# Optimization experiments

Hardware: AMD Instinct MI355X
Metric: run time of the kernel (lower is better)

Reference implementation:

```python
import math
import jax, jax.numpy as jnp
import numpy as np

N_HEADS = 16
D_KV = 64
NUM_BUCKETS = 32
MAX_DISTANCE = 128


def _relative_position_bucket(relative_position, num_buckets=NUM_BUCKETS, max_distance=MAX_DISTANCE):
    # bidirectional=True (encoder)
    num_buckets //= 2
    n = -relative_position
    ret = (n < 0).astype(jnp.int32) * num_buckets
    n = jnp.abs(n)
    max_exact = num_buckets // 2
    is_small = n < max_exact
    val_if_large = max_exact + (
        jnp.log(jnp.maximum(n, 1).astype(jnp.float32) / max_exact)
        / math.log(max_distance / max_exact)
        * (num_buckets - max_exact)
    ).astype(jnp.int32)
    val_if_large = jnp.minimum(val_if_large, num_buckets - 1)
    return ret + jnp.where(is_small, n, val_if_large)


def setup_inputs() -> dict:
    key = jax.random.key(0)
    ks = jax.random.split(key, 6)
    B, S, D = 2, 2048, 1024
    scale = 0.02  # keep pre-softmax logits in a sane range
    return {
        "x": jax.random.normal(ks[0], (B, S, D), dtype=jnp.float32),
        "Wq": jax.random.normal(ks[1], (D, N_HEADS * D_KV), dtype=jnp.float32) * scale,
        "Wk": jax.random.normal(ks[2], (D, N_HEADS * D_KV), dtype=jnp.float32) * scale,
        "Wv": jax.random.normal(ks[3], (D, N_HEADS * D_KV), dtype=jnp.float32) * scale,
        "Wo": jax.random.normal(ks[4], (N_HEADS * D_KV, D), dtype=jnp.float32) * scale,
        "rel_emb": jax.random.normal(ks[5], (NUM_BUCKETS, N_HEADS), dtype=jnp.float32) * scale,
    }


def reference(x, Wq, Wk, Wv, Wo, rel_emb):
    B, S, D = x.shape
    H, Dk = N_HEADS, D_KV

    def shape(t):  # [B,S,H*Dk] -> [B,H,S,Dk]
        return t.reshape(B, S, H, Dk).transpose(0, 2, 1, 3)

    q = shape(x @ Wq)
    k = shape(x @ Wk)
    v = shape(x @ Wv)

    # NOTE: T5 attention has NO 1/sqrt(d) scaling.
    scores = jnp.einsum("bhqd,bhkd->bhqk", q, k)

    # relative position bias: [1, H, S, S]
    ctx_pos = jnp.arange(S)[:, None]
    mem_pos = jnp.arange(S)[None, :]
    rp_bucket = _relative_position_bucket(mem_pos - ctx_pos)  # [S, S]
    position_bias = rel_emb[rp_bucket].transpose(2, 0, 1)[None]  # [1,H,S,S]

    weights = jax.nn.softmax(scores + position_bias, axis=-1)
    context = jnp.einsum("bhqk,bhkd->bhqd", weights, v)
    context = context.transpose(0, 2, 1, 3).reshape(B, S, H * Dk)
    return context @ Wo
```

## Files before the change

### kernel.cpp

```cpp
#include <hip/hip_runtime.h>
#include <math.h>

typedef unsigned short u16;
typedef unsigned int u32;
typedef __attribute__((ext_vector_type(8))) short bf16x8_t;
typedef __attribute__((ext_vector_type(4))) float f32x4_t;
typedef __attribute__((ext_vector_type(16))) float f32x16_t;

#define S_LEN  2048
#define NH     16
#define DK     64
#define DMODEL 1024
#define MROWS  4096
#define LOG2E  1.44269504088896f

__device__ inline u16 f2b(float f) {
  union { float f; u32 u; } c; c.f = f;
  u32 u = c.u;
  return (u16)((u + 0x7fffu + ((u >> 16) & 1u)) >> 16);
}

__device__ __forceinline__ float fexp2(float x) {
#if __has_builtin(__builtin_amdgcn_exp2f)
  return __builtin_amdgcn_exp2f(x);
#else
  return exp2f(x);
#endif
}

__device__ __forceinline__ u32 cvtpk(float lo, float hi) {
  u32 r;
  asm("v_cvt_pk_bf16_f32 %0, %1, %2" : "=v"(r) : "v"(lo), "v"(hi));
  return r;
}

__device__ __forceinline__ void plswap(u32 &x, u32 &y) {
  asm("v_permlane32_swap_b32 %0, %1" : "+v"(x), "+v"(y));
}

__device__ __forceinline__ void stage16(const u16* gp_lane, u16* lds_base) {
#if __has_builtin(__builtin_amdgcn_global_load_lds)
  __builtin_amdgcn_global_load_lds((const __attribute__((address_space(1))) u32*)gp_lane,
                                   (__attribute__((address_space(3))) u32*)lds_base, 16, 0, 0);
#else
  *(uint4*)(lds_base + (threadIdx.x & 63) * 8) = *(const uint4*)gp_lane;
#endif
}

__global__ void prep_kernel(const float* __restrict__ x,
                            const float* __restrict__ Wq, const float* __restrict__ Wk,
                            const float* __restrict__ Wv, const float* __restrict__ Wo,
                            const float* __restrict__ rel,
                            u16* __restrict__ xb, u16* __restrict__ Wall,
                            u16* __restrict__ Wto, float* __restrict__ btab) {
  __shared__ float tile[32][33];
  const int bid = blockIdx.x, t = threadIdx.x;
  if (bid < 4096) {
    int i = (bid * 256 + t) * 4;
    float4 v = *(const float4*)(x + i);
    ushort4 o;
    o.x = f2b(v.x); o.y = f2b(v.y); o.z = f2b(v.z); o.w = f2b(v.w);
    *(ushort4*)(xb + i) = o;
  } else if (bid < 8192) {
    int bid2 = bid - 4096;
    int z = bid2 >> 10, rem = bid2 & 1023;
    const float* W; u16* Wt;
    switch (z) {
      case 0: W = Wq; Wt = Wall; break;
      case 1: W = Wk; Wt = Wall + (size_t)DMODEL * DMODEL; break;
      case 2: W = Wv; Wt = Wall + (size_t)2 * DMODEL * DMODEL; break;
      default: W = Wo; Wt = Wto; break;
    }
    int bc = (rem & 31) * 32, br = (rem >> 5) * 32;
    int tx = t & 31, ty = t >> 5;
    #pragma unroll
    for (int yy = 0; yy < 32; yy += 8)
      tile[ty + yy][tx] = W[(size_t)(br + ty + yy) * DMODEL + bc + tx];
    __syncthreads();
    #pragma unroll
    for (int yy = 0; yy < 32; yy += 8)
      Wt[(size_t)(bc + ty + yy) * DMODEL + br + tx] = f2b(tile[tx][ty + yy]);
  } else {
    int idx = (bid - 8192) * 256 + t;
    if (idx < NH * 4095) {
      int h = idx / 4095;
      int dpos = idx - h * 4095;
      int delta = dpos - 2047;
      int ret = (delta > 0) ? 16 : 0;
      int n = delta < 0 ? -delta : delta;
      int bucket;
      if (n < 8) {
        bucket = ret + n;
      } else {
        float vf = logf((float)n * 0.125f) / 2.7725887222397811f * 8.0f;
        int vil = 8 + (int)vf;
        bucket = ret + (vil < 15 ? vil : 15);
      }
      btab[idx] = (rel[bucket * NH + h] - 16.0f) * LOG2E;
    }
  }
}

#define GSTR 56
template <int MODE>
__global__ __launch_bounds__(256) void gemm128_kernel(const u16* __restrict__ A,
                                                      const u16* __restrict__ Bt,
                                                      float* __restrict__ C,
                                                      u16* __restrict__ q16,
                                                      u16* __restrict__ k16,
                                                      u16* __restrict__ vt16) {
  constexpr int ABSZ = (MODE == 1) ? 4608 : 128 * GSTR;
  constexpr int FSTR = (MODE == 1) ? 32 : GSTR;
  __shared__ __align__(16) u16 As[ABSZ];
  __shared__ __align__(16) u16 Bs[ABSZ];
  const int t = threadIdx.x, w = t >> 6, l = t & 63;
  const int c = l & 15, quad = l >> 4;
  const int m0 = blockIdx.x * 128, n0 = blockIdx.y * 128;
  const int wm = (w & 1) * 64, wn = (w >> 1) * 64;

  f32x4_t acc[16] = {};

  if constexpr (MODE == 1) {
    const int sr = l >> 2;
    const int k8 = (l & 3) * 8;
    const u16* Ag0 = A  + (size_t)(m0 + w * 32 + sr) * DMODEL + k8;
    const u16* Ag1 = Ag0 + (size_t)16 * DMODEL;
    const u16* Bg0 = Bt + (size_t)(n0 + w * 32 + sr) * DMODEL + k8;
    const u16* Bg1 = Bg0 + (size_t)16 * DMODEL;
    u16* Al = As + w * 1024;
    u16* Bl = Bs + w * 1024;
    for (int k0 = 0; k0 < DMODEL; k0 += 32) {
      __syncthreads();
      stage16(Ag0 + k0, Al);
      stage16(Ag1 + k0, Al + 512);
      stage16(Bg0 + k0, Bl);
      stage16(Bg1 + k0, Bl + 512);
      __syncthreads();
      bf16x8_t af[4], bfr[4];
      #pragma unroll
      for (int i = 0; i < 4; ++i) {
        af[i]  = *(const bf16x8_t*)(As + (wm + i * 16 + c) * FSTR + quad * 8);
        bfr[i] = *(const bf16x8_t*)(Bs + (wn + i * 16 + c) * FSTR + quad * 8);
      }
      #pragma unroll
      for (int mt = 0; mt < 4; ++mt)
        #pragma unroll
        for (int nt = 0; nt < 4; ++nt)
          acc[mt * 4 + nt] = __builtin_amdgcn_mfma_f32_16x16x32_bf16(af[mt], bfr[nt], acc[mt * 4 + nt], 0, 0, 0);
    }
  } else {
    const int sr = t >> 2;
    const int k8 = (t & 3) * 8;
    const u16* Ag0 = A  + (size_t)(m0 + sr) * DMODEL + k8;
    const u16* Ag1 = Ag0 + (size_t)64 * DMODEL;
    const u16* Bg0 = Bt + (size_t)(n0 + sr) * DMODEL + k8;
    const u16* Bg1 = Bg0 + (size_t)64 * DMODEL;
    u16* Al0 = As + sr * GSTR + k8;
    u16* Al1 = Al0 + 64 * GSTR;
    u16* Bl0 = Bs + sr * GSTR + k8;
    u16* Bl1 = Bl0 + 64 * GSTR;

    uint4 a0 = *(const uint4*)Ag0, a1 = *(const uint4*)Ag1;
    uint4 b0 = *(const uint4*)Bg0, b1 = *(const uint4*)Bg1;
    for (int k0 = 0; k0 < DMODEL; k0 += 32) {
      __syncthreads();
      *(uint4*)Al0 = a0; *(uint4*)Al1 = a1;
      *(uint4*)Bl0 = b0; *(uint4*)Bl1 = b1;
      __syncthreads();
      if (k0 + 32 < DMODEL) {
        a0 = *(const uint4*)(Ag0 + k0 + 32);
        a1 = *(const uint4*)(Ag1 + k0 + 32);
        b0 = *(const uint4*)(Bg0 + k0 + 32);
        b1 = *(const uint4*)(Bg1 + k0 + 32);
      }
      bf16x8_t af[4], bfr[4];
      #pragma unroll
      for (int i = 0; i < 4; ++i) {
        af[i]  = *(const bf16x8_t*)(As + (wm + i * 16 + c) * FSTR + quad * 8);
        bfr[i] = *(const bf16x8_t*)(Bs + (wn + i * 16 + c) * FSTR + quad * 8);
      }
      #pragma unroll
      for (int mt = 0; mt < 4; ++mt)
        #pragma unroll
        for (int nt = 0; nt < 4; ++nt)
          acc[mt * 4 + nt] = __builtin_amdgcn_mfma_f32_16x16x32_bf16(af[mt], bfr[nt], acc[mt * 4 + nt], 0, 0, 0);
    }
  }

  if constexpr (MODE == 0) {
    #pragma unroll
    for (int mt = 0; mt < 4; ++mt) {
      int grow0 = m0 + wm + mt * 16 + quad * 4;
      #pragma unroll
      for (int nt = 0; nt < 4; ++nt) {
        int gcol = n0 + wn + nt * 16 + c;
        #pragma unroll
        for (int r = 0; r < 4; ++r)
          C[(size_t)(grow0 + r) * DMODEL + gcol] = acc[mt * 4 + nt][r];
      }
    }
  } else {
    const int whichblk = n0 >> 10;
    if (whichblk == 2) {
      #pragma unroll
      for (int mt = 0; mt < 4; ++mt) {
        int grow0 = m0 + wm + mt * 16 + quad * 4;
        int b = grow0 >> 11, s0 = grow0 & 2047;
        #pragma unroll
        for (int nt = 0; nt < 4; ++nt) {
          int cc = (n0 + wn + nt * 16 + c) & 1023;
          int hh = cc >> 6, dk = cc & 63;
          f32x4_t v4 = acc[mt * 4 + nt];
          ushort4 o;
          o.x = f2b(v4[0]); o.y = f2b(v4[1]); o.z = f2b(v4[2]); o.w = f2b(v4[3]);
          *(ushort4*)(vt16 + (((size_t)(b * NH + hh)) * DK + dk) * S_LEN + s0) = o;
        }
      }
    } else {
      u16* tb = (w & 1) ? Bs : As;
      const int base_mw = m0 + wm;
      const int bb = base_mw >> 11, s0g = base_mw & 2047;
      const int cc = (n0 + wn) & 1023;
      const int hh = cc >> 6;
      u16* qk = (whichblk == 0 ? q16 : k16) + (((size_t)(bb * NH + hh)) * S_LEN + s0g) * DK;
      __syncthreads();
      #pragma unroll
      for (int round = 0; round < 2; ++round) {
        if ((w >> 1) == round) {
          #pragma unroll
          for (int mt = 0; mt < 4; ++mt)
            #pragma unroll
            for (int nt = 0; nt < 4; ++nt)
              #pragma unroll
              for (int r = 0; r < 4; ++r)
                tb[(mt * 16 + quad * 4 + r) * 72 + nt * 16 + c] = f2b(acc[mt * 4 + nt][r]);
          #pragma unroll
          for (int i = 0; i < 8; ++i) {
            int lrow = i * 8 + (l >> 3);
            int chk = l & 7;
            uint4 vv = *(const uint4*)(tb + lrow * 72 + chk * 8);
            *(uint4*)(qk + (size_t)lrow * DK + chk * 8) = vv;
          }
        }
        __syncthreads();
      }
    }
  }
}

#define KSTR 72
#define VSTR 136
__global__ __launch_bounds__(512, 4) void attn_mfma_kernel(const u16* __restrict__ q,
                                                           const u16* __restrict__ k,
                                                           const u16* __restrict__ vt,
                                                           const float* __restrict__ btab,
                                                           u16* __restrict__ ctx) {
  __shared__ __align__(16) char smem[37376];
  u16*   Ks   = (u16*)smem;
  u16*   Vts  = (u16*)(smem + 18432);
  float* band = (float*)(smem + 35840);
  float* lpx  = (float*)(smem + 36864);

  const int t = threadIdx.x;
  const int w = t >> 6, l = t & 63;
  const int c32 = l & 31, h32 = l >> 5;
  const int grp = w >> 1, kh = w & 1;

  const int orig = blockIdx.x;
  const int swz = (orig & 7) * 64 + (orig >> 3);
  const int bh = swz >> 4;
  const int q0 = (swz & 15) * 128;
  const int h = bh & (NH - 1), b = bh >> 4;

  const u16* qb = q + (size_t)bh * S_LEN * DK;
  const u16* kb = k + (size_t)bh * S_LEN * DK;
  const u16* vb = vt + (size_t)bh * DK * S_LEN;
  const float* btp = btab + h * 4095 + (2047 - 127 - q0);

  bf16x8_t qfrag[4];
  {
    const u16* qp = qb + (size_t)(q0 + grp * 32 + c32) * DK + h32 * 8;
    qfrag[0] = *(const bf16x8_t*)(qp);
    qfrag[1] = *(const bf16x8_t*)(qp + 16);
    qfrag[2] = *(const bf16x8_t*)(qp + 32);
    qfrag[3] = *(const bf16x8_t*)(qp + 48);
  }

  float lp = 0.f;
  f32x16_t O0 = {}, O1 = {};

  const int ksr = t >> 2;
  const int ksc = (t & 3) * 8;
  const u16* kgp = kb + (size_t)ksr * DK + ksc;
  u16* Kl = Ks + ksr * KSTR + ksc;
  const int vsr = t >> 3;
  const int vsc = (t & 7) * 8;
  const u16* vgp = vb + (size_t)vsr * S_LEN + vsc;
  u16* Vl = Vts + vsr * VSTR + vsc;

  uint4 kr0 = *(const uint4*)kgp;
  uint4 kr1 = *(const uint4*)(kgp + 32);
  uint4 vr0 = *(const uint4*)vgp;
  uint4 vr1 = *(const uint4*)(vgp + 64);
  float br = (t < 256) ? btp[t] : 0.f;

  const int krA = (kh * 64 + c32) * KSTR + h32 * 8;
  const int bndcA = 127 + kh * 64 + 4 * h32 - grp * 32 - c32;

  for (int kt = 0; kt < S_LEN; kt += 128) {
    *(uint4*)Kl = kr0;        *(uint4*)(Kl + 32) = kr1;
    *(uint4*)Vl = vr0;        *(uint4*)(Vl + 64) = vr1;
    if (t < 256) band[t] = br;
    __syncthreads();
    if (kt + 128 < S_LEN) {
      kr0 = *(const uint4*)(kgp + (size_t)(kt + 128) * DK);
      kr1 = *(const uint4*)(kgp + (size_t)(kt + 128) * DK + 32);
      vr0 = *(const uint4*)(vgp + (kt + 128));
      vr1 = *(const uint4*)(vgp + (kt + 128) + 64);
      br = (t < 256) ? btp[kt + 128 + t] : 0.f;
    }
    const int D = kt - q0;
    const bool far = (D >= 256) || (D <= -256);

    f32x16_t sA = {}, sB = {};
    __builtin_amdgcn_s_setprio(1);
    #pragma unroll
    for (int kb4 = 0; kb4 < 4; ++kb4) {
      bf16x8_t kfA = *(const bf16x8_t*)(Ks + krA + kb4 * 16);
      sA = __builtin_amdgcn_mfma_f32_32x32x16_bf16(kfA, qfrag[kb4], sA, 0, 0, 0);
    }
    #pragma unroll
    for (int kb4 = 0; kb4 < 4; ++kb4) {
      bf16x8_t kfB = *(const bf16x8_t*)(Ks + krA + 32 * KSTR + kb4 * 16);
      sB = __builtin_amdgcn_mfma_f32_32x32x16_bf16(kfB, qfrag[kb4], sB, 0, 0, 0);
    }
    __builtin_amdgcn_s_setprio(0);

    const float bfc = band[127];

    {
      float p[16];
      if (far) {
        #pragma unroll
        for (int r = 0; r < 16; ++r)
          p[r] = fexp2(fmaf(sA[r], LOG2E, bfc));
      } else {
        #pragma unroll
        for (int r = 0; r < 16; ++r)
          p[r] = fexp2(fmaf(sA[r], LOG2E, band[bndcA + (r & 3) + 8 * (r >> 2)]));
      }
      #pragma unroll
      for (int r = 0; r < 16; ++r)
        lp += p[r];
      union PW { u32 wds[4]; bf16x8_t v; } pa0, pa1;
      u32 x, y;
      x = cvtpk(p[0], p[1]);   y = cvtpk(p[4], p[5]);   plswap(x, y);
      pa0.wds[0] = x; pa0.wds[2] = y;
      x = cvtpk(p[2], p[3]);   y = cvtpk(p[6], p[7]);   plswap(x, y);
      pa0.wds[1] = x; pa0.wds[3] = y;
      x = cvtpk(p[8], p[9]);   y = cvtpk(p[12], p[13]); plswap(x, y);
      pa1.wds[0] = x; pa1.wds[2] = y;
      x = cvtpk(p[10], p[11]); y = cvtpk(p[14], p[15]); plswap(x, y);
      pa1.wds[1] = x; pa1.wds[3] = y;
      __builtin_amdgcn_s_setprio(1);
      bf16x8_t vf00 = *(const bf16x8_t*)(Vts + (c32)      * VSTR + kh * 64 + h32 * 8);
      bf16x8_t vf01 = *(const bf16x8_t*)(Vts + (32 + c32) * VSTR + kh * 64 + h32 * 8);
      O0 = __builtin_amdgcn_mfma_f32_32x32x16_bf16(pa0.v, vf00, O0, 0, 0, 0);
      O1 = __builtin_amdgcn_mfma_f32_32x32x16_bf16(pa0.v, vf01, O1, 0, 0, 0);
      bf16x8_t vf10 = *(const bf16x8_t*)(Vts + (c32)      * VSTR + kh * 64 + 16 + h32 * 8);
      bf16x8_t vf11 = *(const bf16x8_t*)(Vts + (32 + c32) * VSTR + kh * 64 + 16 + h32 * 8);
      O0 = __builtin_amdgcn_mfma_f32_32x32x16_bf16(pa1.v, vf10, O0, 0, 0, 0);
      O1 = __builtin_amdgcn_mfma_f32_32x32x16_bf16(pa1.v, vf11, O1, 0, 0, 0);
      __builtin_amdgcn_s_setprio(0);
    }

    {
      float p[16];
      if (far) {
        #pragma unroll
        for (int r = 0; r < 16; ++r)
          p[r] = fexp2(fmaf(sB[r], LOG2E, bfc));
      } else {
        #pragma unroll
        for (int r = 0; r < 16; ++r)
          p[r] = fexp2(fmaf(sB[r], LOG2E, band[bndcA + 32 + (r & 3) + 8 * (r >> 2)]));
      }
      #pragma unroll
      for (int r = 0; r < 16; ++r)
        lp += p[r];
      union PW { u32 wds[4]; bf16x8_t v; } pa0, pa1;
      u32 x, y;
      x = cvtpk(p[0], p[1]);   y = cvtpk(p[4], p[5]);   plswap(x, y);
      pa0.wds[0] = x; pa0.wds[2] = y;
      x = cvtpk(p[2], p[3]);   y = cvtpk(p[6], p[7]);   plswap(x, y);
      pa0.wds[1] = x; pa0.wds[3] = y;
      x = cvtpk(p[8], p[9]);   y = cvtpk(p[12], p[13]); plswap(x, y);
      pa1.wds[0] = x; pa1.wds[2] = y;
      x = cvtpk(p[10], p[11]); y = cvtpk(p[14], p[15]); plswap(x, y);
      pa1.wds[1] = x; pa1.wds[3] = y;
      __builtin_amdgcn_s_setprio(1);
      bf16x8_t vf00 = *(const bf16x8_t*)(Vts + (c32)      * VSTR + kh * 64 + 32 + h32 * 8);
      bf16x8_t vf01 = *(const bf16x8_t*)(Vts + (32 + c32) * VSTR + kh * 64 + 32 + h32 * 8);
      O0 = __builtin_amdgcn_mfma_f32_32x32x16_bf16(pa0.v, vf00, O0, 0, 0, 0);
      O1 = __builtin_amdgcn_mfma_f32_32x32x16_bf16(pa0.v, vf01, O1, 0, 0, 0);
      bf16x8_t vf10 = *(const bf16x8_t*)(Vts + (c32)      * VSTR + kh * 64 + 48 + h32 * 8);
      bf16x8_t vf11 = *(const bf16x8_t*)(Vts + (32 + c32) * VSTR + kh * 64 + 48 + h32 * 8);
      O0 = __builtin_amdgcn_mfma_f32_32x32x16_bf16(pa1.v, vf10, O0, 0, 0, 0);
      O1 = __builtin_amdgcn_mfma_f32_32x32x16_bf16(pa1.v, vf11, O1, 0, 0, 0);
      __builtin_amdgcn_s_setprio(0);
    }
    __syncthreads();
  }

  lp += __shfl_xor(lp, 32, 64);
  float (*Ored)[64][33] = (float (*)[64][33])smem;

  if (kh == 1) {
    #pragma unroll
    for (int r = 0; r < 16; ++r) {
      Ored[grp][l][r]      = O0[r];
      Ored[grp][l][16 + r] = O1[r];
    }
    if (l < 32) lpx[grp * 32 + l] = lp;
  }
  __syncthreads();
  if (kh == 0) {
    lp += lpx[grp * 32 + c32];
    float rv = 1.0f / lp;
    #pragma unroll
    for (int r = 0; r < 16; ++r) {
      int qr = (r & 3) + 8 * (r >> 2) + 4 * h32;
      float inv = __shfl(rv, qr, 64);
      float o0 = O0[r] + Ored[grp][l][r];
      float o1 = O1[r] + Ored[grp][l][16 + r];
      int s = q0 + grp * 32 + qr;
      u16* cp = ctx + ((size_t)(b * S_LEN + s)) * DMODEL + h * DK;
      cp[c32]      = f2b(o0 * inv);
      cp[32 + c32] = f2b(o1 * inv);
    }
  }
}

extern "C" void kernel_launch(void* const* d_in, const int* in_sizes, int n_in,
                              void* d_out, int out_size, void* d_ws, size_t ws_size,
                              hipStream_t stream) {
  const float* x   = (const float*)d_in[0];
  const float* Wq  = (const float*)d_in[1];
  const float* Wk  = (const float*)d_in[2];
  const float* Wv  = (const float*)d_in[3];
  const float* Wo  = (const float*)d_in[4];
  const float* rel = (const float*)d_in[5];
  float* out = (float*)d_out;

  char* ws = (char*)d_ws;
  size_t off = 0;
  auto carve = [&](size_t bytes) -> char* {
    char* p = ws + off;
    off += (bytes + 255) & ~(size_t)255;
    return p;
  };
  u16*   xb   = (u16*)  carve((size_t)MROWS * DMODEL * 2);
  u16*   Wall = (u16*)  carve((size_t)3 * DMODEL * DMODEL * 2);
  u16*   Wto  = (u16*)  carve((size_t)DMODEL * DMODEL * 2);
  u16*   qb16 = (u16*)  carve((size_t)4194304 * 2);
  u16*   kb16 = (u16*)  carve((size_t)4194304 * 2);
  u16*   vt16 = (u16*)  carve((size_t)4194304 * 2);
  float* btab = (float*)carve(((size_t)NH * 4095 + 256) * 4);
  u16*   ctxb = (u16*)  carve((size_t)4194304 * 2);

  prep_kernel<<<8448, 256, 0, stream>>>(x, Wq, Wk, Wv, Wo, rel, xb, Wall, Wto, btab);

  dim3 qkvgrid(32, 24);
  gemm128_kernel<1><<<qkvgrid, 256, 0, stream>>>(xb, Wall, nullptr, qb16, kb16, vt16);

  attn_mfma_kernel<<<512, 512, 0, stream>>>(qb16, kb16, vt16, btab, ctxb);

  dim3 ogrid(32, 8);
  gemm128_kernel<0><<<ogrid, 256, 0, stream>>>(ctxb, Wto, out, nullptr, nullptr, nullptr);
}
```

Baseline: 185.1 us.

## Split attention keys four ways per block with 64-query tiles and doubled grid

The attention kernel now handles 64 query rows per block instead of 128. Each query group of 32 rows is served by four waves that each take a 32-key slice of every 128-key tile, and the launch uses 1024 blocks with an occupancy hint of 8. A two-stage shared-memory reduction combines the four partial outputs and row sums, and the far-band test is adjusted for the smaller query range. The aim is more resident blocks and better latency hiding. The cost is that each K/V tile is loaded and staged by twice as many blocks, each wave keeps fewer independent MFMA chains, and the epilogue gains an extra reduction step and barrier.

```diff
diff --git a/kernel.cpp b/kernel.cpp
--- a/kernel.cpp
+++ b/kernel.cpp
@@ -250,12 +250,12 @@
 
 #define KSTR 72
 #define VSTR 136
-__global__ __launch_bounds__(512, 4) void attn_mfma_kernel(const u16* __restrict__ q,
+__global__ __launch_bounds__(512, 8) void attn_mfma_kernel(const u16* __restrict__ q,
                                                            const u16* __restrict__ k,
                                                            const u16* __restrict__ vt,
                                                            const float* __restrict__ btab,
                                                            u16* __restrict__ ctx) {
-  __shared__ __align__(16) char smem[37376];
+  __shared__ __align__(16) char smem[37888];
   u16*   Ks   = (u16*)smem;
   u16*   Vts  = (u16*)(smem + 18432);
   float* band = (float*)(smem + 35840);
@@ -264,12 +264,12 @@
   const int t = threadIdx.x;
   const int w = t >> 6, l = t & 63;
   const int c32 = l & 31, h32 = l >> 5;
-  const int grp = w >> 1, kh = w & 1;
+  const int grp = w >> 2, kq = w & 3;
 
   const int orig = blockIdx.x;
-  const int swz = (orig & 7) * 64 + (orig >> 3);
-  const int bh = swz >> 4;
-  const int q0 = (swz & 15) * 128;
+  const int swz = (orig & 7) * 128 + (orig >> 3);
+  const int bh = swz >> 5;
+  const int q0 = (swz & 31) * 64;
   const int h = bh & (NH - 1), b = bh >> 4;
 
   const u16* qb = q + (size_t)bh * S_LEN * DK;
@@ -304,8 +304,8 @@
   uint4 vr1 = *(const uint4*)(vgp + 64);
   float br = (t < 256) ? btp[t] : 0.f;
 
-  const int krA = (kh * 64 + c32) * KSTR + h32 * 8;
-  const int bndcA = 127 + kh * 64 + 4 * h32 - grp * 32 - c32;
+  const int krA = (kq * 32 + c32) * KSTR + h32 * 8;
+  const int bndcA = 127 + kq * 32 + 4 * h32 - grp * 32 - c32;
 
   for (int kt = 0; kt < S_LEN; kt += 128) {
     *(uint4*)Kl = kr0;        *(uint4*)(Kl + 32) = kr1;
@@ -320,39 +320,34 @@
       br = (t < 256) ? btp[kt + 128 + t] : 0.f;
     }
     const int D = kt - q0;
-    const bool far = (D >= 256) || (D <= -256);
-
-    f32x16_t sA = {}, sB = {};
+    const bool far = (D >= 192) || (D <= -256);
+
+    f32x16_t s4 = {};
     __builtin_amdgcn_s_setprio(1);
     #pragma unroll
     for (int kb4 = 0; kb4 < 4; ++kb4) {
-      bf16x8_t kfA = *(const bf16x8_t*)(Ks + krA + kb4 * 16);
-      sA = __builtin_amdgcn_mfma_f32_32x32x16_bf16(kfA, qfrag[kb4], sA, 0, 0, 0);
-    }
-    #pragma unroll
-    for (int kb4 = 0; kb4 < 4; ++kb4) {
-      bf16x8_t kfB = *(const bf16x8_t*)(Ks + krA + 32 * KSTR + kb4 * 16);
-      sB = __builtin_amdgcn_mfma_f32_32x32x16_bf16(kfB, qfrag[kb4], sB, 0, 0, 0);
+      bf16x8_t kf = *(const bf16x8_t*)(Ks + krA + kb4 * 16);
+      s4 = __builtin_amdgcn_mfma_f32_32x32x16_bf16(kf, qfrag[kb4], s4, 0, 0, 0);
     }
     __builtin_amdgcn_s_setprio(0);
 
-    const float bfc = band[127];
-
+    float p[16];
+    if (far) {
+      const float bfc = band[127];
+      #pragma unroll
+      for (int r = 0; r < 16; ++r)
+        p[r] = fexp2(fmaf(s4[r], LOG2E, bfc));
+    } else {
+      #pragma unroll
+      for (int r = 0; r < 16; ++r)
+        p[r] = fexp2(fmaf(s4[r], LOG2E, band[bndcA + (r & 3) + 8 * (r >> 2)]));
+    }
+    #pragma unroll
+    for (int r = 0; r < 16; ++r)
+      lp += p[r];
+
+    union PW { u32 wds[4]; bf16x8_t v; } pa0, pa1;
     {
-      float p[16];
-      if (far) {
-        #pragma unroll
-        for (int r = 0; r < 16; ++r)
-          p[r] = fexp2(fmaf(sA[r], LOG2E, bfc));
-      } else {
-        #pragma unroll
-        for (int r = 0; r < 16; ++r)
-          p[r] = fexp2(fmaf(sA[r], LOG2E, band[bndcA + (r & 3) + 8 * (r >> 2)]));
-      }
-      #pragma unroll
-      for (int r = 0; r < 16; ++r)
-        lp += p[r];
-      union PW { u32 wds[4]; bf16x8_t v; } pa0, pa1;
       u32 x, y;
       x = cvtpk(p[0], p[1]);   y = cvtpk(p[4], p[5]);   plswap(x, y);
       pa0.wds[0] = x; pa0.wds[2] = y;
@@ -362,81 +357,73 @@
       pa1.wds[0] = x; pa1.wds[2] = y;
       x = cvtpk(p[10], p[11]); y = cvtpk(p[14], p[15]); plswap(x, y);
       pa1.wds[1] = x; pa1.wds[3] = y;
-      __builtin_amdgcn_s_setprio(1);
-      bf16x8_t vf00 = *(const bf16x8_t*)(Vts + (c32)      * VSTR + kh * 64 + h32 * 8);
-      bf16x8_t vf01 = *(const bf16x8_t*)(Vts + (32 + c32) * VSTR + kh * 64 + h32 * 8);
+    }
+
+    __builtin_amdgcn_s_setprio(1);
+    {
+      bf16x8_t vf00 = *(const bf16x8_t*)(Vts + (c32)      * VSTR + kq * 32 + h32 * 8);
+      bf16x8_t vf01 = *(const bf16x8_t*)(Vts + (32 + c32) * VSTR + kq * 32 + h32 * 8);
       O0 = __builtin_amdgcn_mfma_f32_32x32x16_bf16(pa0.v, vf00, O0, 0, 0, 0);
       O1 = __builtin_amdgcn_mfma_f32_32x32x16_bf16(pa0.v, vf01, O1, 0, 0, 0);
-      bf16x8_t vf10 = *(const bf16x8_t*)(Vts + (c32)      * VSTR + kh * 64 + 16 + h32 * 8);
-      bf16x8_t vf11 = *(const bf16x8_t*)(Vts + (32 + c32) * VSTR + kh * 64 + 16 + h32 * 8);
+      bf16x8_t vf10 = *(const bf16x8_t*)(Vts + (c32)      * VSTR + kq * 32 + 16 + h32 * 8);
+      bf16x8_t vf11 = *(const bf16x8_t*)(Vts + (32 + c32) * VSTR + kq * 32 + 16 + h32 * 8);
       O0 = __builtin_amdgcn_mfma_f32_32x32x16_bf16(pa1.v, vf10, O0, 0, 0, 0);
       O1 = __builtin_amdgcn_mfma_f32_32x32x16_bf16(pa1.v, vf11, O1, 0, 0, 0);
-      __builtin_amdgcn_s_setprio(0);
-    }
-
-    {
-      float p[16];
-      if (far) {
-        #pragma unroll
-        for (int r = 0; r < 16; ++r)
-          p[r] = fexp2(fmaf(sB[r], LOG2E, bfc));
-      } else {
-        #pragma unroll
-        for (int r = 0; r < 16; ++r)
-          p[r] = fexp2(fmaf(sB[r], LOG2E, band[bndcA + 32 + (r & 3) + 8 * (r >> 2)]));
-      }
-      #pragma unroll
-      for (int r = 0; r < 16; ++r)
-        lp += p[r];
-      union PW { u32 wds[4]; bf16x8_t v; } pa0, pa1;
-      u32 x, y;
-      x = cvtpk(p[0], p[1]);   y = cvtpk(p[4], p[5]);   plswap(x, y);
-      pa0.wds[0] = x; pa0.wds[2] = y;
-      x = cvtpk(p[2], p[3]);   y = cvtpk(p[6], p[7]);   plswap(x, y);
-      pa0.wds[1] = x; pa0.wds[3] = y;
-      x = cvtpk(p[8], p[9]);   y = cvtpk(p[12], p[13]); plswap(x, y);
-      pa1.wds[0] = x; pa1.wds[2] = y;
-      x = cvtpk(p[10], p[11]); y = cvtpk(p[14], p[15]); plswap(x, y);
-      pa1.wds[1] = x; pa1.wds[3] = y;
-      __builtin_amdgcn_s_setprio(1);
-      bf16x8_t vf00 = *(const bf16x8_t*)(Vts + (c32)      * VSTR + kh * 64 + 32 + h32 * 8);
-      bf16x8_t vf01 = *(const bf16x8_t*)(Vts + (32 + c32) * VSTR + kh * 64 + 32 + h32 * 8);
-      O0 = __builtin_amdgcn_mfma_f32_32x32x16_bf16(pa0.v, vf00, O0, 0, 0, 0);
-      O1 = __builtin_amdgcn_mfma_f32_32x32x16_bf16(pa0.v, vf01, O1, 0, 0, 0);
-      bf16x8_t vf10 = *(const bf16x8_t*)(Vts + (c32)      * VSTR + kh * 64 + 48 + h32 * 8);
-      bf16x8_t vf11 = *(const bf16x8_t*)(Vts + (32 + c32) * VSTR + kh * 64 + 48 + h32 * 8);
-      O0 = __builtin_amdgcn_mfma_f32_32x32x16_bf16(pa1.v, vf10, O0, 0, 0, 0);
-      O1 = __builtin_amdgcn_mfma_f32_32x32x16_bf16(pa1.v, vf11, O1, 0, 0, 0);
-      __builtin_amdgcn_s_setprio(0);
-    }
+    }
+    __builtin_amdgcn_s_setprio(0);
     __syncthreads();
   }
 
   lp += __shfl_xor(lp, 32, 64);
-  float (*Ored)[64][33] = (float (*)[64][33])smem;
-
-  if (kh == 1) {
-    #pragma unroll
-    for (int r = 0; r < 16; ++r) {
-      Ored[grp][l][r]      = O0[r];
-      Ored[grp][l][16 + r] = O1[r];
-    }
-    if (l < 32) lpx[grp * 32 + l] = lp;
-  }
+  float (*Ored)[2][64][33] = (float (*)[2][64][33])smem;
+
+  if (kq == 1 || kq == 3) {
+    const int slot = kq >> 1;
+    #pragma unroll
+    for (int r = 0; r < 16; ++r) {
+      Ored[grp][slot][l][r]      = O0[r];
+      Ored[grp][slot][l][16 + r] = O1[r];
+    }
+  }
+  if (kq != 0 && l < 32) lpx[(grp * 4 + kq) * 32 + l] = lp;
   __syncthreads();
-  if (kh == 0) {
-    lp += lpx[grp * 32 + c32];
+
+  if (kq == 0) {
+    #pragma unroll
+    for (int r = 0; r < 16; ++r) {
+      O0[r] += Ored[grp][0][l][r];
+      O1[r] += Ored[grp][0][l][16 + r];
+    }
+  } else if (kq == 2) {
+    #pragma unroll
+    for (int r = 0; r < 16; ++r) {
+      O0[r] += Ored[grp][1][l][r];
+      O1[r] += Ored[grp][1][l][16 + r];
+    }
+    #pragma unroll
+    for (int r = 0; r < 16; ++r) {
+      Ored[grp][1][l][r]      = O0[r];
+      Ored[grp][1][l][16 + r] = O1[r];
+    }
+  }
+  __syncthreads();
+
+  if (kq == 0) {
+    #pragma unroll
+    for (int r = 0; r < 16; ++r) {
+      O0[r] += Ored[grp][1][l][r];
+      O1[r] += Ored[grp][1][l][16 + r];
+    }
+    lp += lpx[(grp * 4 + 1) * 32 + c32] + lpx[(grp * 4 + 2) * 32 + c32] + lpx[(grp * 4 + 3) * 32 + c32];
     float rv = 1.0f / lp;
     #pragma unroll
     for (int r = 0; r < 16; ++r) {
       int qr = (r & 3) + 8 * (r >> 2) + 4 * h32;
       float inv = __shfl(rv, qr, 64);
-      float o0 = O0[r] + Ored[grp][l][r];
-      float o1 = O1[r] + Ored[grp][l][16 + r];
       int s = q0 + grp * 32 + qr;
       u16* cp = ctx + ((size_t)(b * S_LEN + s)) * DMODEL + h * DK;
-      cp[c32]      = f2b(o0 * inv);
-      cp[32 + c32] = f2b(o1 * inv);
+      cp[c32]      = f2b(O0[r] * inv);
+      cp[32 + c32] = f2b(O1[r] * inv);
     }
   }
 }
@@ -473,7 +460,7 @@
   dim3 qkvgrid(32, 24);
   gemm128_kernel<1><<<qkvgrid, 256, 0, stream>>>(xb, Wall, nullptr, qb16, kb16, vt16);
 
-  attn_mfma_kernel<<<512, 512, 0, stream>>>(qb16, kb16, vt16, btab, ctxb);
+  attn_mfma_kernel<<<1024, 512, 0, stream>>>(qb16, kb16, vt16, btab, ctxb);
 
   dim3 ogrid(32, 8);
   gemm128_kernel<0><<<ogrid, 256, 0, stream>>>(ctxb, Wto, out, nullptr, nullptr, nullptr);
```

Measured after the change: 537.1 us. 2.9x slower.
